# Performance work log

Measured on AMD Instinct MI355X. Metric: run time of the kernel, lower is better.

The kernel has to match this reference:

```python
import jax, jax.numpy as jnp
import numpy as np

EPS = 1e-5
C = 128
B = 16384
SYMBIOTIC = 4.0
NUM_PARENTS = 16
CHILDREN_PER_PARENT = 7


def _inverse(v):
    # torch: sort -> rank -> reversed rank -> gather sorted values
    idx0 = np.argsort(v, kind='stable')
    value = v[idx0]
    idx1 = np.argsort(idx0, kind='stable')  # ranks
    idx2 = v.shape[0] - 1 - idx1
    return value[idx2]


def _build_stats():
    counts = np.floor(50000.0 * 0.97 ** np.arange(C)) + 1.0  # long-tailed
    N = counts.sum()
    weight = (N / counts).astype(np.float32)
    prior = np.eye(C, dtype=np.float32)
    for p in range(NUM_PARENTS):
        ch = NUM_PARENTS + CHILDREN_PER_PARENT * p + np.arange(CHILDREN_PER_PARENT)
        prior[p, ch] = 1.0
    prior_me = (prior == 0).astype(np.float32)          # 1 - prior, keep only exact 1s
    prior_ms = prior - np.eye(C, dtype=np.float32)      # prior (0/1) minus eye
    v1_sig = np.log(N / counts - 1.0 + EPS).astype(np.float32)
    v2_sig = _inverse(v1_sig).astype(np.float32)
    v1_sm = np.log(counts / N + EPS).astype(np.float32)
    v2_sm = _inverse(v1_sm).astype(np.float32)
    return weight, prior_me, prior_ms, v1_sig, v2_sig, v1_sm, v2_sm


def setup_inputs() -> dict:
    key = jax.random.key(0)
    k1, k2 = jax.random.split(key)
    weight, prior_me, prior_ms, v1s, v2s, v1m, v2m = _build_stats()
    logits = 0.5 * jax.random.normal(k1, (12, B, C), dtype=jnp.float32)
    target = (jax.random.uniform(k2, (B, C)) < 0.1).astype(jnp.float32)
    return {
        'logits': logits, 'target': target,
        'weight': jnp.asarray(weight),
        'prior_me': jnp.asarray(prior_me), 'prior_ms': jnp.asarray(prior_ms),
        'v1_sigmoid': jnp.asarray(v1s), 'v2_sigmoid': jnp.asarray(v2s),
        'v1_softmax': jnp.asarray(v1m), 'v2_softmax': jnp.asarray(v2m),
    }


def reference(logits, target, weight, prior_me, prior_ms,
              v1_sigmoid, v2_sigmoid, v1_softmax, v2_softmax):
    zero = jnp.zeros_like(v1_sigmoid)
    # experts 0-5: sigmoid variants (long-tailed / balanced / inversed, twice)
    sig_shift = jnp.stack([zero, v1_sigmoid, v1_sigmoid - v2_sigmoid] * 2)  # [6,C]
    a_sig = jax.nn.sigmoid(logits[:6] - sig_shift[:, None, :])
    # experts 6-11: local-softmax variants
    sm_shift = jnp.stack([zero, v1_softmax, v1_softmax - v2_softmax] * 2)   # [6,C]
    e = jnp.exp(logits[6:] + sm_shift[:, None, :])                          # [6,B,C]
    denom = jnp.einsum('ebc,cd->ebd', e, prior_me) + e
    a_sm = e / (denom + EPS)
    acti = jnp.clip(jnp.concatenate([a_sig, a_sm], axis=0), EPS, 1.0 - EPS)  # [12,B,C]
    # weighted BCE per expert, summed
    bce = -weight * (target * jnp.log(acti) + (1.0 - target) * jnp.log(1.0 - acti))
    loss = jnp.sum(jnp.mean(bce, axis=(1, 2)))
    # symbiotic regularizer on experts 3,4,5,9,10,11
    row_sum = jnp.sum(prior_ms, axis=1)                 # [C]
    n_nz = jnp.sum(row_sum > 0).astype(acti.dtype)
    bsz = acti.shape[1]

    def symb(a):  # a: [B,C] activated logits
        def step(acc, xs):
            mask_row, parent = xs                       # [C], [B]
            term = jnp.log1p(jnp.exp(a - parent[:, None]))  # [B,C]
            rs = jnp.sum(mask_row)
            contrib = jnp.where(rs > 0, jnp.sum(term * mask_row) / (bsz * rs), 0.0)
            return acc + contrib, None
        total, _ = jax.lax.scan(step, jnp.float32(0.0), (prior_ms, a.T))
        return total / n_nz

    reg = jax.vmap(symb)(acti[jnp.array([3, 4, 5, 9, 10, 11])])
    return loss + SYMBIOTIC * jnp.sum(reg)
```

## Files before the change

kernel.cpp:

```cpp
#include <hip/hip_runtime.h>
#include <math.h>

#define CC 128
#define BB 16384
#define MEPS 1e-5f
#define NBLK 2048


__global__ __launch_bounds__(256) void mel_main(
    const float* __restrict__ logits, const float* __restrict__ target,
    const float* __restrict__ weight,
    const float* __restrict__ v1s, const float* __restrict__ v2s,
    const float* __restrict__ v1m, const float* __restrict__ v2m,
    float* __restrict__ partial)
{
    const int lane = threadIdx.x & 63;
    const int wib  = threadIdx.x >> 6;
    const int wave = blockIdx.x * 4 + wib;
    const int r    = lane >> 5;
    const int c    = lane & 31;
    const int row  = wave * 2 + r;

    const float4 wtv = ((const float4*)weight)[c];
    const float4 s1v = ((const float4*)v1s)[c];
    const float4 s2v = ((const float4*)v2s)[c];
    const float4 m1v = ((const float4*)v1m)[c];
    const float4 m2v = ((const float4*)v2m)[c];
    const float wt[4] = {wtv.x, wtv.y, wtv.z, wtv.w};
    const float sv[3][4] = {{0.f,0.f,0.f,0.f},
                            {s1v.x, s1v.y, s1v.z, s1v.w},
                            {s1v.x-s2v.x, s1v.y-s2v.y, s1v.z-s2v.z, s1v.w-s2v.w}};
    const float mv[3][4] = {{0.f,0.f,0.f,0.f},
                            {m1v.x, m1v.y, m1v.z, m1v.w},
                            {m1v.x-m2v.x, m1v.y-m2v.y, m1v.z-m2v.z, m1v.w-m2v.w}};

    const float childf = (c >= 4) ? 1.f : 0.f;
    int pidx[4];
    #pragma unroll
    for (int k = 0; k < 4; ++k) {
        const int ch = 4*c + k;
        pidx[k] = (ch >= 16) ? (ch - 16) / 7 : 0;
    }

    float tg[4], xs[6][4], xm[6][4];
    {
        const size_t ro = (size_t)row * CC;
        const float4 t4 = ((const float4*)(target + ro))[c];
        tg[0]=t4.x; tg[1]=t4.y; tg[2]=t4.z; tg[3]=t4.w;
        #pragma unroll
        for (int e = 0; e < 6; ++e) {
            const float4 v = ((const float4*)(logits + (size_t)e*(size_t)BB*CC + ro))[c];
            xs[e][0]=v.x; xs[e][1]=v.y; xs[e][2]=v.z; xs[e][3]=v.w;
        }
        #pragma unroll
        for (int j = 0; j < 6; ++j) {
            const float4 v = ((const float4*)(logits + (size_t)(6+j)*(size_t)BB*CC + ro))[c];
            xm[j][0]=v.x; xm[j][1]=v.y; xm[j][2]=v.z; xm[j][3]=v.w;
        }
    }

    float accP = 0.f;
    float accS = 0.f;

    float ca[3][4];
    #pragma unroll
    for (int e = 0; e < 6; ++e) {
        const int si = e % 3;
        #pragma unroll
        for (int k = 0; k < 4; ++k) {
            const float z  = xs[e][k] - sv[si][k];
            const float ex = __expf(-z);
            const float opx = 1.f + ex;
            const float sp = __logf(opx);
            const float tz = (tg[k] > 0.5f) ? 0.f : z;
            accP = fmaf(wt[k], sp + tz, accP);
            if (e >= 3) ca[e-3][k] = __builtin_amdgcn_rcpf(opx);
        }
    }

    float em[6][4], S[6];
    #pragma unroll
    for (int j = 0; j < 6; ++j) {
        const int si = j % 3;
        #pragma unroll
        for (int k = 0; k < 4; ++k)
            em[j][k] = __expf(xm[j][k] + mv[si][k]);
        S[j] = (em[j][0] + em[j][1]) + (em[j][2] + em[j][3]);
    }

    #pragma unroll
    for (int off = 16; off > 0; off >>= 1) {
        #pragma unroll
        for (int j = 0; j < 6; ++j)
            S[j] += __shfl_xor(S[j], off, 64);
    }

    __shared__ float lds[4][9][2][16];
    if (c < 4) {
        #pragma unroll
        for (int t = 0; t < 3; ++t)
            *(float4*)&lds[wib][t][r][4*c] = make_float4(ca[t][0], ca[t][1], ca[t][2], ca[t][3]);
        #pragma unroll
        for (int j = 0; j < 6; ++j)
            *(float4*)&lds[wib][3+j][r][4*c] = make_float4(em[j][0], em[j][1], em[j][2], em[j][3]);
    }

    #pragma unroll
    for (int t = 0; t < 3; ++t) {
        #pragma unroll
        for (int k = 0; k < 4; ++k) {
            const float cap = lds[wib][t][r][pidx[k]];
            const float d   = ca[t][k] - cap;
            accS = fmaf(childf, __logf(1.f + __expf(d)), accS);
        }
    }

    #pragma unroll
    for (int j = 0; j < 6; ++j) {
        const float Sj = S[j] + MEPS;
        const float rS = __builtin_amdgcn_rcpf(Sj);
        #pragma unroll
        for (int k = 0; k < 4; ++k) {
            const float ep  = lds[wib][3+j][r][pidx[k]];
            const float den = Sj - childf * ep;
            float a = em[j][k] * __builtin_amdgcn_rcpf(den);
            a = fminf(fmaxf(a, MEPS), 1.f - MEPS);
            const float arg = (tg[k] > 0.5f) ? a : 1.f - a;
            accP = fmaf(wt[k], -__logf(arg), accP);
            if (j >= 3) {
                float ap = ep * rS;
                ap = fminf(fmaxf(ap, MEPS), 1.f - MEPS);
                accS = fmaf(childf, __logf(1.f + __expf(a - ap)), accS);
            }
        }
    }

    float val = accP * (1.f / ((float)BB * (float)CC))
              + accS * (4.f / (112.f * (float)BB));

    #pragma unroll
    for (int off = 32; off > 0; off >>= 1)
        val += __shfl_xor(val, off, 64);

    __shared__ float sdata[4];
    if (lane == 0) sdata[wib] = val;
    __syncthreads();
    if (threadIdx.x == 0)
        partial[blockIdx.x] = (sdata[0] + sdata[1]) + (sdata[2] + sdata[3]);
}

__global__ __launch_bounds__(256) void mel_reduce(
    const float* __restrict__ partial, float* __restrict__ out)
{
    float v = 0.f;
    #pragma unroll
    for (int i = 0; i < NBLK / 256; ++i)
        v += partial[threadIdx.x + i * 256];
    #pragma unroll
    for (int off = 32; off > 0; off >>= 1)
        v += __shfl_xor(v, off, 64);
    __shared__ float s[4];
    const int lane = threadIdx.x & 63, wib = threadIdx.x >> 6;
    if (lane == 0) s[wib] = v;
    __syncthreads();
    if (threadIdx.x == 0) out[0] = (s[0] + s[1]) + (s[2] + s[3]);
}

extern "C" void kernel_launch(void* const* d_in, const int* in_sizes, int n_in,
                              void* d_out, int out_size, void* d_ws, size_t ws_size,
                              hipStream_t stream) {
    const float* logits = (const float*)d_in[0];
    const float* target = (const float*)d_in[1];
    const float* weight = (const float*)d_in[2];
    const float* v1s = (const float*)d_in[5];
    const float* v2s = (const float*)d_in[6];
    const float* v1m = (const float*)d_in[7];
    const float* v2m = (const float*)d_in[8];
    float* partial = (float*)d_ws;
    float* out = (float*)d_out;

    mel_main<<<NBLK, 256, 0, stream>>>(logits, target, weight,
                                       v1s, v2s, v1m, v2m, partial);
    mel_reduce<<<1, 256, 0, stream>>>(partial, out);
}
```

Measured before the change: 171.4 us.

## Stream experts in a prefetched loop and use polynomial softplus for symbiotic term

The kernel no longer loads all 12 expert logit vectors up front. It walks the experts in a non-unrolled loop that prefetches the next expert's float4, and reuses one small LDS slot per row for the parent values. The aim is to cut register pressure and LDS use so more waves fit (launch bounds now request 6 waves per EU). The symbiotic log1p(exp(d)) is replaced by an even-order Taylor polynomial, which is valid because d lies in (-1,1). The trade-off is fewer loads in flight per wave, plus a small approximation error and the dropped clamp on the parent softmax activation.

Measured after the change: 166.9 us. 1.03x faster.

```diff
diff --git a/kernel.cpp b/kernel.cpp
--- a/kernel.cpp
+++ b/kernel.cpp
@@ -7,7 +7,14 @@
 #define NBLK 2048
 
 
-__global__ __launch_bounds__(256) void mel_main(
+__device__ __forceinline__ float softplus1(float d) {
+    const float u = d * d;
+    float p = fmaf(u, 3.4722222e-4f, -5.2083333e-3f);
+    p = fmaf(u, p, 0.125f);
+    return fmaf(u, p, fmaf(d, 0.5f, 0.69314718f));
+}
+
+__global__ __launch_bounds__(256, 6) void mel_main(
     const float* __restrict__ logits, const float* __restrict__ target,
     const float* __restrict__ weight,
     const float* __restrict__ v1s, const float* __restrict__ v2s,
@@ -20,119 +27,91 @@
     const int r    = lane >> 5;
     const int c    = lane & 31;
     const int row  = wave * 2 + r;
+    const size_t ro = (size_t)row * CC;
 
-    const float4 wtv = ((const float4*)weight)[c];
+    const float4 wt4 = ((const float4*)weight)[c];
     const float4 s1v = ((const float4*)v1s)[c];
     const float4 s2v = ((const float4*)v2s)[c];
     const float4 m1v = ((const float4*)v1m)[c];
     const float4 m2v = ((const float4*)v2m)[c];
-    const float wt[4] = {wtv.x, wtv.y, wtv.z, wtv.w};
-    const float sv[3][4] = {{0.f,0.f,0.f,0.f},
-                            {s1v.x, s1v.y, s1v.z, s1v.w},
-                            {s1v.x-s2v.x, s1v.y-s2v.y, s1v.z-s2v.z, s1v.w-s2v.w}};
-    const float mv[3][4] = {{0.f,0.f,0.f,0.f},
-                            {m1v.x, m1v.y, m1v.z, m1v.w},
-                            {m1v.x-m2v.x, m1v.y-m2v.y, m1v.z-m2v.z, m1v.w-m2v.w}};
+    const float4 tv  = ((const float4*)(target + ro))[c];
+
+    const float wt[4] = {wt4.x, wt4.y, wt4.z, wt4.w};
+    const float s1[4] = {s1v.x, s1v.y, s1v.z, s1v.w};
+    const float sd[4] = {s1v.x - s2v.x, s1v.y - s2v.y, s1v.z - s2v.z, s1v.w - s2v.w};
+    const float m1[4] = {m1v.x, m1v.y, m1v.z, m1v.w};
+    const float md[4] = {m1v.x - m2v.x, m1v.y - m2v.y, m1v.z - m2v.z, m1v.w - m2v.w};
+    const bool  tb[4] = {tv.x > 0.5f, tv.y > 0.5f, tv.z > 0.5f, tv.w > 0.5f};
 
     const float childf = (c >= 4) ? 1.f : 0.f;
-    int pidx[4];
+    int pofs[4];
     #pragma unroll
     for (int k = 0; k < 4; ++k) {
-        const int ch = 4*c + k;
-        pidx[k] = (ch >= 16) ? (ch - 16) / 7 : 0;
+        const int ch = 4 * c + k;
+        pofs[k] = (ch >= 16) ? (ch - 16) / 7 : 0;
     }
 
-    float tg[4], xs[6][4], xm[6][4];
-    {
-        const size_t ro = (size_t)row * CC;
-        const float4 t4 = ((const float4*)(target + ro))[c];
-        tg[0]=t4.x; tg[1]=t4.y; tg[2]=t4.z; tg[3]=t4.w;
-        #pragma unroll
-        for (int e = 0; e < 6; ++e) {
-            const float4 v = ((const float4*)(logits + (size_t)e*(size_t)BB*CC + ro))[c];
-            xs[e][0]=v.x; xs[e][1]=v.y; xs[e][2]=v.z; xs[e][3]=v.w;
-        }
-        #pragma unroll
-        for (int j = 0; j < 6; ++j) {
-            const float4 v = ((const float4*)(logits + (size_t)(6+j)*(size_t)BB*CC + ro))[c];
-            xm[j][0]=v.x; xm[j][1]=v.y; xm[j][2]=v.z; xm[j][3]=v.w;
-        }
-    }
+    __shared__ float lds[4][2][16];
+    float* Lp = &lds[wib][r][0];
 
+    const float* pp = logits + ro;
+    float4 cur = ((const float4*)pp)[c];
     float accP = 0.f;
     float accS = 0.f;
 
-    float ca[3][4];
-    #pragma unroll
-    for (int e = 0; e < 6; ++e) {
+    #pragma unroll 1
+    for (int e = 0; e < 12; ++e) {
+        float4 nxt = cur;
+        if (e < 11) nxt = ((const float4*)(pp + (size_t)BB * CC))[c];
+        pp += (size_t)BB * CC;
         const int si = e % 3;
-        #pragma unroll
-        for (int k = 0; k < 4; ++k) {
-            const float z  = xs[e][k] - sv[si][k];
-            const float ex = __expf(-z);
-            const float opx = 1.f + ex;
-            const float sp = __logf(opx);
-            const float tz = (tg[k] > 0.5f) ? 0.f : z;
-            accP = fmaf(wt[k], sp + tz, accP);
-            if (e >= 3) ca[e-3][k] = __builtin_amdgcn_rcpf(opx);
-        }
-    }
+        const float x[4] = {cur.x, cur.y, cur.z, cur.w};
 
-    float em[6][4], S[6];
-    #pragma unroll
-    for (int j = 0; j < 6; ++j) {
-        const int si = j % 3;
-        #pragma unroll
-        for (int k = 0; k < 4; ++k)
-            em[j][k] = __expf(xm[j][k] + mv[si][k]);
-        S[j] = (em[j][0] + em[j][1]) + (em[j][2] + em[j][3]);
-    }
-
-    #pragma unroll
-    for (int off = 16; off > 0; off >>= 1) {
-        #pragma unroll
-        for (int j = 0; j < 6; ++j)
-            S[j] += __shfl_xor(S[j], off, 64);
-    }
-
-    __shared__ float lds[4][9][2][16];
-    if (c < 4) {
-        #pragma unroll
-        for (int t = 0; t < 3; ++t)
-            *(float4*)&lds[wib][t][r][4*c] = make_float4(ca[t][0], ca[t][1], ca[t][2], ca[t][3]);
-        #pragma unroll
-        for (int j = 0; j < 6; ++j)
-            *(float4*)&lds[wib][3+j][r][4*c] = make_float4(em[j][0], em[j][1], em[j][2], em[j][3]);
-    }
-
-    #pragma unroll
-    for (int t = 0; t < 3; ++t) {
-        #pragma unroll
-        for (int k = 0; k < 4; ++k) {
-            const float cap = lds[wib][t][r][pidx[k]];
-            const float d   = ca[t][k] - cap;
-            accS = fmaf(childf, __logf(1.f + __expf(d)), accS);
-        }
-    }
-
-    #pragma unroll
-    for (int j = 0; j < 6; ++j) {
-        const float Sj = S[j] + MEPS;
-        const float rS = __builtin_amdgcn_rcpf(Sj);
-        #pragma unroll
-        for (int k = 0; k < 4; ++k) {
-            const float ep  = lds[wib][3+j][r][pidx[k]];
-            const float den = Sj - childf * ep;
-            float a = em[j][k] * __builtin_amdgcn_rcpf(den);
-            a = fminf(fmaxf(a, MEPS), 1.f - MEPS);
-            const float arg = (tg[k] > 0.5f) ? a : 1.f - a;
-            accP = fmaf(wt[k], -__logf(arg), accP);
-            if (j >= 3) {
-                float ap = ep * rS;
-                ap = fminf(fmaxf(ap, MEPS), 1.f - MEPS);
-                accS = fmaf(childf, __logf(1.f + __expf(a - ap)), accS);
+        if (e < 6) {
+            float a[4];
+            #pragma unroll
+            for (int k = 0; k < 4; ++k) {
+                const float sh = (si == 0) ? 0.f : ((si == 1) ? s1[k] : sd[k]);
+                const float z  = x[k] - sh;
+                const float ex = __expf(-z);
+                const float sp = __logf(1.f + ex);
+                accP = fmaf(wt[k], sp + (tb[k] ? 0.f : z), accP);
+                a[k] = __builtin_amdgcn_rcpf(1.f + ex);
+            }
+            if (e >= 3) {
+                if (c < 4) *(float4*)(Lp + 4 * c) = make_float4(a[0], a[1], a[2], a[3]);
+                #pragma unroll
+                for (int k = 0; k < 4; ++k)
+                    accS = fmaf(childf, softplus1(a[k] - Lp[pofs[k]]), accS);
+            }
+        } else {
+            float ek[4];
+            float S = 0.f;
+            #pragma unroll
+            for (int k = 0; k < 4; ++k) {
+                const float sh = (si == 0) ? 0.f : ((si == 1) ? m1[k] : md[k]);
+                ek[k] = __expf(x[k] + sh);
+                S += ek[k];
+            }
+            #pragma unroll
+            for (int off = 16; off > 0; off >>= 1)
+                S += __shfl_xor(S, off, 64);
+            const float Sj = S + MEPS;
+            if (c < 4) *(float4*)(Lp + 4 * c) = make_float4(ek[0], ek[1], ek[2], ek[3]);
+            const float rS = __builtin_amdgcn_rcpf(Sj);
+            #pragma unroll
+            for (int k = 0; k < 4; ++k) {
+                const float ep  = Lp[pofs[k]];
+                const float den = Sj - childf * ep;
+                float a = ek[k] * __builtin_amdgcn_rcpf(den);
+                a = fminf(fmaxf(a, MEPS), 1.f - MEPS);
+                const float arg = tb[k] ? a : 1.f - a;
+                accP = fmaf(wt[k], -__logf(arg), accP);
+                if (e >= 9)
+                    accS = fmaf(childf, softplus1(a - ep * rS), accS);
             }
         }
+        cur = nxt;
     }
 
     float val = accP * (1.f / ((float)BB * (float)CC))
```
